# Kernel tuning notes

Hardware: AMD Instinct MI355X
Metric: run time of the kernel (lower is better)

Reference implementation:

```python
import jax, jax.numpy as jnp
import numpy as np

B, C, H, W = 16, 64, 128, 128
C8 = C // 8


def setup_inputs() -> dict:
    key = jax.random.key(0)
    ks = jax.random.split(key, 8)
    s = 0.05
    return {
        "x": jax.random.normal(ks[0], (B, C, H, W), dtype=jnp.float32),
        "Wq": jax.random.normal(ks[1], (C8, C), dtype=jnp.float32) * s,
        "bq": jax.random.normal(ks[2], (C8,), dtype=jnp.float32) * s,
        "Wk": jax.random.normal(ks[3], (C8, C), dtype=jnp.float32) * s,
        "bk": jax.random.normal(ks[4], (C8,), dtype=jnp.float32) * s,
        "Wv": jax.random.normal(ks[5], (C, C), dtype=jnp.float32) * s,
        "bv": jax.random.normal(ks[6], (C,), dtype=jnp.float32) * s,
        "gamma": jnp.zeros((1,), dtype=jnp.float32),
    }


def _criss_cross(x, Wq, bq, Wk, bk, Wv, bv, gamma):
    # 1x1 convs == channel-mixing matmuls
    q = jnp.einsum("bchw,oc->bohw", x, Wq) + bq[None, :, None, None]  # [B,C8,H,W]
    k = jnp.einsum("bchw,oc->bohw", x, Wk) + bk[None, :, None, None]  # [B,C8,H,W]
    v = jnp.einsum("bchw,oc->bohw", x, Wv) + bv[None, :, None, None]  # [B,C,H,W]

    h = x.shape[2]
    # column (H-axis) attention scores; diagonal masked to -inf
    energy_H = jnp.einsum("bchw,bciw->bhwi", q, k)  # [B,H,W,H]
    diag = jnp.eye(h, dtype=bool)[None, :, None, :]  # mask where query row == key row
    energy_H = jnp.where(diag, -jnp.inf, energy_H)
    # row (W-axis) attention scores
    energy_W = jnp.einsum("bchw,bchj->bhwj", q, k)  # [B,H,W,W]

    # joint softmax over concatenated H+W axis
    att = jax.nn.softmax(jnp.concatenate([energy_H, energy_W], axis=3), axis=3)
    att_H = att[:, :, :, :h]    # [B,H,W,H]
    att_W = att[:, :, :, h:]    # [B,H,W,W]

    out_H = jnp.einsum("bhwi,bciw->bchw", att_H, v)
    out_W = jnp.einsum("bhwj,bchj->bchw", att_W, v)
    return gamma[0] * (out_H + out_W) + x


def reference(x, Wq, bq, Wk, bk, Wv, bv, gamma):
    return _criss_cross(x, Wq, bq, Wk, bk, Wv, bv, gamma)
```

## Files before the change

kernel.cpp:

```cpp
#include <hip/hip_runtime.h>

#define HW 128
#define CC 64
#define C8V 8
#define NB 16
#define LOG2E 1.44269504088896f

typedef _Float16 h1;
typedef _Float16 h2 __attribute__((ext_vector_type(2)));
typedef _Float16 half8 __attribute__((ext_vector_type(8)));
typedef float float16v __attribute__((ext_vector_type(16)));
typedef uint uv4 __attribute__((ext_vector_type(4)));

__device__ __forceinline__ uint packh2(float a, float b) {
#if __has_builtin(__builtin_amdgcn_cvt_pkrtz)
  return __builtin_bit_cast(uint, __builtin_amdgcn_cvt_pkrtz(a, b));
#else
  h2 v; v[0] = (h1)a; v[1] = (h1)b; return __builtin_bit_cast(uint, v);
#endif
}
__device__ __forceinline__ ushort f2h(float a) { h1 v = (h1)a; return __builtin_bit_cast(ushort, v); }
__device__ __forceinline__ float  h2f(ushort a) { return (float)__builtin_bit_cast(h1, a); }

__device__ __forceinline__ float fexp2(float x) {
#if __has_builtin(__builtin_amdgcn_exp2f)
  return __builtin_amdgcn_exp2f(x);
#else
  return exp2f(x);
#endif
}

__device__ __forceinline__ float16v mfma16(uv4 a, uv4 b, float16v c) {
  return __builtin_amdgcn_mfma_f32_32x32x16_f16(
      __builtin_bit_cast(half8, a), __builtin_bit_cast(half8, b), c, 0, 0, 0);
}

__global__ __launch_bounds__(256) void k_prep(
    const float* __restrict__ Wq, const float* __restrict__ bq,
    const float* __restrict__ Wk, const float* __restrict__ bk,
    const float* __restrict__ Wv, const float* __restrict__ bv,
    ushort* __restrict__ W_frag, float* __restrict__ bias_f)
{
  int idx = blockIdx.x * 256 + threadIdx.x;
  if (idx < 6144) {
    int g = idx >> 3, e = idx & 7;
    int kshi = g / 96, o = g % 96;
    int ks = kshi >> 1, hi = kshi & 1;
    int c = 8 * hi + 16 * ks + e;
    float val = (o < 8)  ? Wq[o * 64 + c] * LOG2E
              : (o < 16) ? Wk[(o - 8) * 64 + c]
              : (o < 80) ? Wv[(o - 16) * 64 + c] : 0.f;
    W_frag[idx] = f2h(val);
  }
  if (blockIdx.x == 0 && threadIdx.x < 96) {
    int t = threadIdx.x;
    bias_f[t] = (t < 8) ? bq[t] * LOG2E : (t < 16) ? bk[t - 8] : (t < 80) ? bv[t - 16] : 0.f;
  }
}

__global__ __launch_bounds__(256, 4) void k_projW(
    const float* __restrict__ x, const ushort* __restrict__ W_frag,
    const float* __restrict__ bias_f,
    ushort* __restrict__ qT, ushort* __restrict__ kT,
    ushort* __restrict__ v,
    ushort* __restrict__ oW_, float* __restrict__ mW_, float* __restrict__ sW_)
{
  alignas(16) __shared__ uint V_l[64 * 64];
  alignas(16) __shared__ ushort qk_l[128 * 24];
  __shared__ float bias_l[96];

  int t = threadIdx.x;
  int lane = t & 63, wv = t >> 6, hi = lane >> 5;
  int b = blockIdx.x >> 7, r = blockIdx.x & 127;
  if (t < 96) bias_l[t] = bias_f[t];

  int w = 32 * wv + (lane & 31);
  const float* xw = x + (size_t)(b * CC) * (HW * HW) + (size_t)r * HW + w;
  const size_t PL = (size_t)HW * HW;

  float16v acc0 = {}, acc1 = {}, acc2 = {};
  #pragma unroll
  for (int ks = 0; ks < 4; ++ks) {
    int c0 = 8 * hi + 16 * ks;
    uint bx[4];
    #pragma unroll
    for (int e2 = 0; e2 < 4; ++e2) {
      float f0 = xw[(size_t)(c0 + 2 * e2) * PL];
      float f1 = xw[(size_t)(c0 + 2 * e2 + 1) * PL];
      bx[e2] = packh2(f0, f1);
    }
    uv4 Bx = {bx[0], bx[1], bx[2], bx[3]};
    const ushort* wf = W_frag + (size_t)(ks * 2 + hi) * 96 * 8;
    uv4 a0 = *(const uv4*)(wf + (lane & 31) * 8);
    uv4 a1 = *(const uv4*)(wf + ((lane & 31) + 32) * 8);
    uv4 a2 = *(const uv4*)(wf + ((lane & 31) + 64) * 8);
    acc0 = mfma16(a0, Bx, acc0);
    acc1 = mfma16(a1, Bx, acc1);
    acc2 = mfma16(a2, Bx, acc2);
  }
  __syncthreads();

  #pragma unroll
  for (int reg = 0; reg < 16; ++reg) {
    int orow = (reg & 3) + 8 * (reg >> 2) + 4 * hi;
    float v0 = acc0[reg] + bias_l[orow];
    if (orow < 16) {
      qk_l[w * 24 + orow] = f2h(v0);
    } else {
      int c = orow - 16;
      *(ushort*)((char*)V_l + c * 256 + ((2 * w) ^ ((c & 15) << 4))) = f2h(v0);
    }
    int c1 = orow + 16;
    *(ushort*)((char*)V_l + c1 * 256 + ((2 * w) ^ ((c1 & 15) << 4))) =
        f2h(acc1[reg] + bias_l[orow + 32]);
    if (orow < 16) {
      int c2_ = orow + 48;
      *(ushort*)((char*)V_l + c2_ * 256 + ((2 * w) ^ ((c2_ & 15) << 4))) =
          f2h(acc2[reg] + bias_l[orow + 64]);
    }
  }
  __syncthreads();

  ushort* vb = v + (size_t)(b * CC) * PL + (size_t)r * HW;
  #pragma unroll
  for (int i = 0; i < 4; ++i) {
    int idx = t + 256 * i; int c = idx >> 4, j8 = idx & 15;
    uv4 val = *(const uv4*)((const char*)V_l + c * 256 + ((16 * j8) ^ ((c & 15) << 4)));
    *(uv4*)(vb + (size_t)c * PL + j8 * 8) = val;
  }
  {
    int pix = t & 127, isk = t >> 7;
    uv4 val = *(const uv4*)&qk_l[pix * 24 + isk * 8];
    ushort* dstt = (isk ? kT : qT) + ((size_t)(b * HW + pix) * HW + r) * 8;
    *(uv4*)dstt = val;
  }

  int qg = w;
  uv4 Bq = {0, 0, 0, 0};
  uv4 ka[4] = {{0,0,0,0}, {0,0,0,0}, {0,0,0,0}, {0,0,0,0}};
  if (hi == 0) {
    Bq = *(const uv4*)&qk_l[qg * 24];
    #pragma unroll
    for (int mt = 0; mt < 4; ++mt)
      ka[mt] = *(const uv4*)&qk_l[((lane & 31) + 32 * mt) * 24 + 8];
  }

  float16v e[4];
  #pragma unroll
  for (int mt = 0; mt < 4; ++mt) {
    float16v z = {};
    e[mt] = mfma16(ka[mt], Bq, z);
  }

  float m = -INFINITY;
  #pragma unroll
  for (int mt = 0; mt < 4; ++mt)
    #pragma unroll
    for (int reg = 0; reg < 16; reg += 2)
      m = fmaxf(m, fmaxf(e[mt][reg], e[mt][reg + 1]));
  m = fmaxf(m, __shfl_xor(m, 32));

  float s0 = 0.f, s1 = 0.f, s2 = 0.f, s3 = 0.f;
  #pragma unroll
  for (int mt = 0; mt < 4; ++mt) {
    #pragma unroll
    for (int reg = 0; reg < 16; reg += 4) {
      float p0 = fexp2(e[mt][reg + 0] - m);
      float p1 = fexp2(e[mt][reg + 1] - m);
      float p2 = fexp2(e[mt][reg + 2] - m);
      float p3 = fexp2(e[mt][reg + 3] - m);
      e[mt][reg + 0] = p0; e[mt][reg + 1] = p1;
      e[mt][reg + 2] = p2; e[mt][reg + 3] = p3;
      s0 += p0; s1 += p1; s2 += p2; s3 += p3;
    }
  }
  float s = (s0 + s1) + (s2 + s3);
  s += __shfl_xor(s, 32);
  if (lane < 32) {
    mW_[(size_t)blockIdx.x * HW + qg] = m;
    sW_[(size_t)blockIdx.x * HW + qg] = s;
  }

  float16v pacc0 = {}, pacc1 = {};
  #pragma unroll
  for (int s8 = 0; s8 < 8; ++s8) {
    int mt = s8 >> 1, hf = s8 & 1;
    float p0 = e[mt][8 * hf + 0], p1 = e[mt][8 * hf + 1];
    float p2 = e[mt][8 * hf + 2], p3 = e[mt][8 * hf + 3];
    float p4 = e[mt][8 * hf + 4], p5 = e[mt][8 * hf + 5];
    float p6 = e[mt][8 * hf + 6], p7 = e[mt][8 * hf + 7];
    uint X = packh2(p0, p1), Y = packh2(p2, p3), Z = packh2(p4, p5), Wp = packh2(p6, p7);
    uint Xs = __shfl_xor(X, 32), Ys = __shfl_xor(Y, 32);
    uint Zs = __shfl_xor(Z, 32), Ws = __shfl_xor(Wp, 32);
    uv4 Bp;
    Bp[0] = (hi == 0) ? X  : Zs;
    Bp[1] = (hi == 0) ? Y  : Ws;
    Bp[2] = (hi == 0) ? Xs : Z;
    Bp[3] = (hi == 0) ? Ys : Wp;
    #pragma unroll
    for (int ct = 0; ct < 2; ++ct) {
      int c = (lane & 31) + 32 * ct;
      uint byteoff = c * 256 + ((16 * (hi + 2 * s8)) ^ ((c & 15) << 4));
      uv4 va = *(const uv4*)((const char*)V_l + byteoff);
      if (ct == 0) pacc0 = mfma16(va, Bp, pacc0);
      else         pacc1 = mfma16(va, Bp, pacc1);
    }
  }

  __syncthreads();
  ushort* o_l = (ushort*)V_l;
  #pragma unroll
  for (int reg = 0; reg < 16; ++reg) {
    int c = (reg & 3) + 8 * (reg >> 2) + 4 * hi;
    o_l[(c +  0) * 128 + w] = f2h(pacc0[reg]);
    o_l[(c + 32) * 128 + w] = f2h(pacc1[reg]);
  }
  __syncthreads();
  ushort* ob = oW_ + (size_t)(b * CC) * PL + (size_t)r * HW;
  #pragma unroll
  for (int i = 0; i < 4; ++i) {
    int idx = t + 256 * i; int c = idx >> 4, w8 = idx & 15;
    *(uv4*)(ob + (size_t)c * PL + w8 * 8) = *(const uv4*)&o_l[c * 128 + w8 * 8];
  }
}

__global__ __launch_bounds__(256) void k_transpose_v(const ushort* __restrict__ v,
                                                     ushort* __restrict__ vT)
{
  __shared__ ushort tl[128 * 130];
  int t = threadIdx.x;
  size_t base = (size_t)blockIdx.x * (HW * HW);
  const uint* ip = (const uint*)(v + base);
  uint* op = (uint*)(vT + base);
  int c2 = t & 63;
  int r0 = t >> 6;
  for (int it = 0; it < 32; ++it) {
    int r = it * 4 + r0;
    uint val = ip[r * 64 + c2];
    *(uint*)&tl[r * 130 + c2 * 2] = val;
  }
  __syncthreads();
  for (int it = 0; it < 32; ++it) {
    int wcol = it * 4 + r0;
    int hh = c2 * 2;
    uint lo = tl[hh * 130 + wcol];
    uint hi = tl[(hh + 1) * 130 + wcol];
    op[wcol * 64 + c2] = lo | (hi << 16);
  }
}

__global__ __launch_bounds__(256, 4) void k_attnH(
    const ushort* __restrict__ qT, const ushort* __restrict__ kT,
    const ushort* __restrict__ vT,
    ushort* __restrict__ oH_, float* __restrict__ mH_, float* __restrict__ sH_)
{
  alignas(16) __shared__ uint V_l[64 * 64];

  int t = threadIdx.x;
  int lane = t & 63, wv = t >> 6;
  int hi = lane >> 5;
  int bid = blockIdx.x;
  int b = bid >> 7, r = bid & 127;
  size_t plane32 = (size_t)(HW * HW) / 2;
  size_t pixbase = (size_t)(b * HW + r) * HW * 8;

  int qg = 32 * wv + (lane & 31);
  uv4 Bq = {0, 0, 0, 0};
  uv4 ka[4] = {{0,0,0,0}, {0,0,0,0}, {0,0,0,0}, {0,0,0,0}};
  if (hi == 0) {
    Bq = *(const uv4*)(qT + pixbase + (size_t)qg * 8);
    #pragma unroll
    for (int mt = 0; mt < 4; ++mt)
      ka[mt] = *(const uv4*)(kT + pixbase + (size_t)((lane & 31) + 32 * mt) * 8);
  }

  const uint* vrow = (const uint*)vT + (size_t)(b * CC) * plane32 + (size_t)r * 64;
  #pragma unroll
  for (int i = 0; i < 4; ++i) {
    int idx = t + 256 * i; int c = idx >> 4, j4 = idx & 15;
    uv4 val = *(const uv4*)(vrow + (size_t)c * plane32 + 4 * j4);
    uint byteoff = c * 256 + ((16 * j4) ^ ((c & 15) << 4));
    *(uv4*)((char*)V_l + byteoff) = val;
  }
  __syncthreads();

  float16v e[4];
  #pragma unroll
  for (int mt = 0; mt < 4; ++mt) {
    float16v z = {};
    e[mt] = mfma16(ka[mt], Bq, z);
  }

  #pragma unroll
  for (int mt = 0; mt < 4; ++mt)
    #pragma unroll
    for (int reg = 0; reg < 16; ++reg) {
      int key = 32 * mt + ((reg & 3) + 8 * (reg >> 2) + 4 * hi);
      e[mt][reg] = (key == qg) ? -INFINITY : e[mt][reg];
    }

  float m = -INFINITY;
  #pragma unroll
  for (int mt = 0; mt < 4; ++mt)
    #pragma unroll
    for (int reg = 0; reg < 16; reg += 2)
      m = fmaxf(m, fmaxf(e[mt][reg], e[mt][reg + 1]));
  m = fmaxf(m, __shfl_xor(m, 32));

  float s0 = 0.f, s1 = 0.f, s2 = 0.f, s3 = 0.f;
  #pragma unroll
  for (int mt = 0; mt < 4; ++mt) {
    #pragma unroll
    for (int reg = 0; reg < 16; reg += 4) {
      float p0 = fexp2(e[mt][reg + 0] - m);
      float p1 = fexp2(e[mt][reg + 1] - m);
      float p2 = fexp2(e[mt][reg + 2] - m);
      float p3 = fexp2(e[mt][reg + 3] - m);
      e[mt][reg + 0] = p0; e[mt][reg + 1] = p1;
      e[mt][reg + 2] = p2; e[mt][reg + 3] = p3;
      s0 += p0; s1 += p1; s2 += p2; s3 += p3;
    }
  }
  float s = (s0 + s1) + (s2 + s3);
  s += __shfl_xor(s, 32);
  if (lane < 32) {
    mH_[(size_t)bid * HW + qg] = m;
    sH_[(size_t)bid * HW + qg] = s;
  }

  float16v acc0 = {}, acc1 = {};
  #pragma unroll
  for (int s8 = 0; s8 < 8; ++s8) {
    int mt = s8 >> 1, hf = s8 & 1;
    float p0 = e[mt][8 * hf + 0], p1 = e[mt][8 * hf + 1];
    float p2 = e[mt][8 * hf + 2], p3 = e[mt][8 * hf + 3];
    float p4 = e[mt][8 * hf + 4], p5 = e[mt][8 * hf + 5];
    float p6 = e[mt][8 * hf + 6], p7 = e[mt][8 * hf + 7];
    uint X = packh2(p0, p1), Y = packh2(p2, p3), Z = packh2(p4, p5), Wp = packh2(p6, p7);
    uint Xs = __shfl_xor(X, 32), Ys = __shfl_xor(Y, 32);
    uint Zs = __shfl_xor(Z, 32), Ws = __shfl_xor(Wp, 32);
    uv4 Bp;
    Bp[0] = (hi == 0) ? X  : Zs;
    Bp[1] = (hi == 0) ? Y  : Ws;
    Bp[2] = (hi == 0) ? Xs : Z;
    Bp[3] = (hi == 0) ? Ys : Wp;
    #pragma unroll
    for (int ct = 0; ct < 2; ++ct) {
      int c = (lane & 31) + 32 * ct;
      uint byteoff = c * 256 + ((16 * (hi + 2 * s8)) ^ ((c & 15) << 4));
      uv4 va = *(const uv4*)((const char*)V_l + byteoff);
      if (ct == 0) acc0 = mfma16(va, Bp, acc0);
      else         acc1 = mfma16(va, Bp, acc1);
    }
  }

  __syncthreads();
  ushort* o_l = (ushort*)V_l;
  int w = 32 * wv + (lane & 31);
  #pragma unroll
  for (int reg = 0; reg < 16; ++reg) {
    int c = (reg & 3) + 8 * (reg >> 2) + 4 * hi;
    o_l[(c +  0) * 128 + w] = f2h(acc0[reg]);
    o_l[(c + 32) * 128 + w] = f2h(acc1[reg]);
  }
  __syncthreads();
  ushort* ob = oH_ + (size_t)(b * CC) * (HW * HW) + (size_t)r * HW;
  #pragma unroll
  for (int i = 0; i < 4; ++i) {
    int idx = t + 256 * i; int c = idx >> 4, w8 = idx & 15;
    *(uv4*)(ob + (size_t)c * (HW * HW) + w8 * 8) = *(const uv4*)&o_l[c * 128 + w8 * 8];
  }
}

__global__ __launch_bounds__(256) void k_alpha(
    const float* __restrict__ mH, const float* __restrict__ sH,
    const float* __restrict__ mW, const float* __restrict__ sW,
    ushort* __restrict__ aHT, ushort* __restrict__ aWn)
{
  __shared__ float mw_l[128 * 9], sw_l[128 * 9];
  __shared__ ushort aw_l[128 * 10];
  int t = threadIdx.x;
  int b = blockIdx.x >> 4, ws = blockIdx.x & 15;
  int w0 = ws * 8;
  const int PL = HW * HW;

  #pragma unroll
  for (int i = 0; i < 4; ++i) {
    int p = t + 256 * i;
    int w = p & 7, h = p >> 3;
    mw_l[h * 9 + w] = mW[(size_t)b * PL + h * HW + w0 + w];
    sw_l[h * 9 + w] = sW[(size_t)b * PL + h * HW + w0 + w];
  }
  __syncthreads();
  #pragma unroll
  for (int i = 0; i < 4; ++i) {
    int p = t + 256 * i;
    int h = p & 127, w = p >> 7;
    size_t tidx = (size_t)b * PL + (size_t)(w0 + w) * HW + h;
    float mh = mH[tidx], sh = sH[tidx];
    float mw = mw_l[h * 9 + w], sw = sw_l[h * 9 + w];
    float mm = fmaxf(mh, mw);
    float eh = fexp2(mh - mm), ew = fexp2(mw - mm);
    float inv = 1.f / (sh * eh + sw * ew);
    aHT[tidx] = f2h(eh * inv);
    aw_l[h * 10 + w] = f2h(ew * inv);
  }
  __syncthreads();
  #pragma unroll
  for (int i = 0; i < 4; ++i) {
    int p = t + 256 * i;
    int w = p & 7, h = p >> 3;
    aWn[(size_t)b * PL + (size_t)h * HW + w0 + w] = aw_l[h * 10 + w];
  }
}

__global__ __launch_bounds__(256) void k_merge(
    const ushort* __restrict__ oHT, const ushort* __restrict__ oW,
    const ushort* __restrict__ aHT, const ushort* __restrict__ aWn,
    const float* __restrict__ x, const float* __restrict__ gamma,
    float* __restrict__ out)
{
  alignas(16) __shared__ ushort otile[2 * 32 * 132];
  int t = threadIdx.x;
  int bid = blockIdx.x;
  int wsel = bid & 3, cg = (bid >> 2) & 31, b = bid >> 7;
  int w0 = wsel * 32;
  float g = gamma[0];
  const int PL = HW * HW;

  #pragma unroll
  for (int i = 0; i < 4; ++i) {
    int p = t + 256 * i;
    int ch = p >> 9, rest = p & 511;
    int w = rest >> 4, hg = rest & 15;
    size_t cbase = (size_t)(b * CC + cg * 2 + ch) * PL;
    uv4 ov = *(const uv4*)(oHT + cbase + (size_t)(w0 + w) * HW + hg * 8);
    uv4 av = *(const uv4*)(aHT + (size_t)b * PL + (size_t)(w0 + w) * HW + hg * 8);
    uv4 res;
    #pragma unroll
    for (int jj = 0; jj < 4; ++jj) {
      h2 o2 = __builtin_bit_cast(h2, ov[jj]);
      h2 a2 = __builtin_bit_cast(h2, av[jj]);
      res[jj] = __builtin_bit_cast(uint, o2 * a2);
    }
    *(uv4*)&otile[(ch * 32 + w) * 132 + hg * 8] = res;
  }
  __syncthreads();

  #pragma unroll
  for (int ch = 0; ch < 2; ++ch) {
    size_t cbase = (size_t)(b * CC + cg * 2 + ch) * PL;
    const ushort* otc = &otile[ch * 32 * 132];
    #pragma unroll
    for (int i = 0; i < 2; ++i) {
      int p = t + 256 * i;
      int w4 = p & 7, hh2 = p >> 3;
      float th0[4], th1[4];
      #pragma unroll
      for (int j = 0; j < 4; ++j) {
        uint pk = *(const uint*)&otc[(4 * w4 + j) * 132 + 2 * hh2];
        th0[j] = h2f((ushort)(pk & 0xffff));
        th1[j] = h2f((ushort)(pk >> 16));
      }
      #pragma unroll
      for (int rr = 0; rr < 2; ++rr) {
        int hh = 2 * hh2 + rr;
        const float* th = rr ? th1 : th0;
        size_t base = cbase + (size_t)hh * HW + w0 + 4 * w4;
        size_t abase = (size_t)b * PL + (size_t)hh * HW + w0 + 4 * w4;
        uint2 aw2 = *(const uint2*)(aWn + abase);
        uint2 ow2 = *(const uint2*)(oW + base);
        float4 xv = *(const float4*)(x + base);
        float4 res;
        res.x = g * (th[0] + h2f((ushort)(ow2.x & 0xffff)) * h2f((ushort)(aw2.x & 0xffff))) + xv.x;
        res.y = g * (th[1] + h2f((ushort)(ow2.x >> 16))    * h2f((ushort)(aw2.x >> 16)))    + xv.y;
        res.z = g * (th[2] + h2f((ushort)(ow2.y & 0xffff)) * h2f((ushort)(aw2.y & 0xffff))) + xv.z;
        res.w = g * (th[3] + h2f((ushort)(ow2.y >> 16))    * h2f((ushort)(aw2.y >> 16)))    + xv.w;
        *(float4*)(out + base) = res;
      }
    }
  }
}

extern "C" void kernel_launch(void* const* d_in, const int* in_sizes, int n_in,
                              void* d_out, int out_size, void* d_ws, size_t ws_size,
                              hipStream_t stream)
{
  const float* x     = (const float*)d_in[0];
  const float* Wq    = (const float*)d_in[1];
  const float* bq    = (const float*)d_in[2];
  const float* Wk    = (const float*)d_in[3];
  const float* bk    = (const float*)d_in[4];
  const float* Wv    = (const float*)d_in[5];
  const float* bv    = (const float*)d_in[6];
  const float* gamma = (const float*)d_in[7];
  float* out = (float*)d_out;

  char* w = (char*)d_ws;
  size_t np = (size_t)NB * HW * HW;
  ushort* W_frag = (ushort*)w; w += 6144 * 2;
  float*  bias_f = (float*)w;  w += 96 * 4 + 320;
  ushort* qT  = (ushort*)w;  w += np * 8 * 2;
  ushort* kT  = (ushort*)w;  w += np * 8 * 2;
  ushort* v   = (ushort*)w;  w += np * CC * 2;
  ushort* vT  = (ushort*)w;  w += np * CC * 2;
  ushort* oW  = (ushort*)w;  w += np * CC * 2;
  ushort* oHT = (ushort*)w;  w += np * CC * 2;
  float* mW = (float*)w;  w += np * 4;
  float* sW = (float*)w;  w += np * 4;
  float* mH = (float*)w;  w += np * 4;
  float* sH = (float*)w;  w += np * 4;
  ushort* aHT = (ushort*)w; w += np * 2;
  ushort* aWn = (ushort*)w; w += np * 2;
  if ((size_t)(w - (char*)d_ws) > ws_size) return;

  k_prep<<<24, 256, 0, stream>>>(Wq, bq, Wk, bk, Wv, bv, W_frag, bias_f);
  k_projW<<<NB * HW, 256, 0, stream>>>(x, W_frag, bias_f, qT, kT, v, oW, mW, sW);
  k_transpose_v<<<NB * CC, 256, 0, stream>>>(v, vT);
  k_attnH<<<NB * HW, 256, 0, stream>>>(qT, kT, vT, oHT, mH, sH);
  k_alpha<<<NB * 16, 256, 0, stream>>>(mH, sH, mW, sW, aHT, aWn);
  k_merge<<<NB * 32 * 4, 256, 0, stream>>>(oHT, oW, aHT, aWn, x, gamma, out);
}
```

Before: 107.4 us.

## Fuse softmax normalization into attnH and drop k_alpha kernel

Computes the joint H/W softmax combine factors directly inside k_attnH using the row-stats mW/sW, scales the H output by its weight before storing, and writes the W weight. This removes the separate k_alpha launch and the mH/sH/aHT buffers and their traffic, and lets k_merge skip the aHT load and multiply. It also hoists global loads in k_projW and k_merge ahead of compute to raise memory-level parallelism, at the cost of more registers. The mW/sW reads in attnH are strided gathers, one element per row.

After: 103.3 us. 1.04x faster.

```diff
diff --git a/kernel.cpp b/kernel.cpp
--- a/kernel.cpp
+++ b/kernel.cpp
@@ -2,7 +2,6 @@
 
 #define HW 128
 #define CC 64
-#define C8V 8
 #define NB 16
 #define LOG2E 1.44269504088896f
 
@@ -78,18 +77,23 @@
   const float* xw = x + (size_t)(b * CC) * (HW * HW) + (size_t)r * HW + w;
   const size_t PL = (size_t)HW * HW;
 
-  float16v acc0 = {}, acc1 = {}, acc2 = {};
+  float xv[32];
   #pragma unroll
   for (int ks = 0; ks < 4; ++ks) {
     int c0 = 8 * hi + 16 * ks;
-    uint bx[4];
-    #pragma unroll
-    for (int e2 = 0; e2 < 4; ++e2) {
-      float f0 = xw[(size_t)(c0 + 2 * e2) * PL];
-      float f1 = xw[(size_t)(c0 + 2 * e2 + 1) * PL];
-      bx[e2] = packh2(f0, f1);
-    }
-    uv4 Bx = {bx[0], bx[1], bx[2], bx[3]};
+    #pragma unroll
+    for (int e = 0; e < 8; ++e)
+      xv[ks * 8 + e] = xw[(size_t)(c0 + e) * PL];
+  }
+  __builtin_amdgcn_sched_barrier(0);
+
+  float16v acc0 = {}, acc1 = {}, acc2 = {};
+  #pragma unroll
+  for (int ks = 0; ks < 4; ++ks) {
+    uv4 Bx;
+    #pragma unroll
+    for (int e2 = 0; e2 < 4; ++e2)
+      Bx[e2] = packh2(xv[ks * 8 + 2 * e2], xv[ks * 8 + 2 * e2 + 1]);
     const ushort* wf = W_frag + (size_t)(ks * 2 + hi) * 96 * 8;
     uv4 a0 = *(const uv4*)(wf + (lane & 31) * 8);
     uv4 a1 = *(const uv4*)(wf + ((lane & 31) + 32) * 8);
@@ -252,7 +256,8 @@
 __global__ __launch_bounds__(256, 4) void k_attnH(
     const ushort* __restrict__ qT, const ushort* __restrict__ kT,
     const ushort* __restrict__ vT,
-    ushort* __restrict__ oH_, float* __restrict__ mH_, float* __restrict__ sH_)
+    const float* __restrict__ mW_, const float* __restrict__ sW_,
+    ushort* __restrict__ oH_, ushort* __restrict__ aWn)
 {
   alignas(16) __shared__ uint V_l[64 * 64];
 
@@ -262,6 +267,7 @@
   int bid = blockIdx.x;
   int b = bid >> 7, r = bid & 127;
   size_t plane32 = (size_t)(HW * HW) / 2;
+  const size_t PL = (size_t)HW * HW;
   size_t pixbase = (size_t)(b * HW + r) * HW * 8;
 
   int qg = 32 * wv + (lane & 31);
@@ -273,6 +279,8 @@
     for (int mt = 0; mt < 4; ++mt)
       ka[mt] = *(const uv4*)(kT + pixbase + (size_t)((lane & 31) + 32 * mt) * 8);
   }
+  float mw = mW_[(size_t)b * PL + (size_t)qg * HW + r];
+  float sw = sW_[(size_t)b * PL + (size_t)qg * HW + r];
 
   const uint* vrow = (const uint*)vT + (size_t)(b * CC) * plane32 + (size_t)r * 64;
   #pragma unroll
@@ -323,10 +331,13 @@
   }
   float s = (s0 + s1) + (s2 + s3);
   s += __shfl_xor(s, 32);
-  if (lane < 32) {
-    mH_[(size_t)bid * HW + qg] = m;
-    sH_[(size_t)bid * HW + qg] = s;
-  }
+
+  float mm = fmaxf(m, mw);
+  float eh = fexp2(m - mm), ew = fexp2(mw - mm);
+  float inv = 1.f / (s * eh + sw * ew);
+  float aH = eh * inv;
+  if (hi == 0)
+    aWn[(size_t)b * PL + (size_t)qg * HW + r] = f2h(ew * inv);
 
   float16v acc0 = {}, acc1 = {};
   #pragma unroll
@@ -360,63 +371,21 @@
   #pragma unroll
   for (int reg = 0; reg < 16; ++reg) {
     int c = (reg & 3) + 8 * (reg >> 2) + 4 * hi;
-    o_l[(c +  0) * 128 + w] = f2h(acc0[reg]);
-    o_l[(c + 32) * 128 + w] = f2h(acc1[reg]);
-  }
-  __syncthreads();
-  ushort* ob = oH_ + (size_t)(b * CC) * (HW * HW) + (size_t)r * HW;
+    o_l[(c +  0) * 128 + w] = f2h(acc0[reg] * aH);
+    o_l[(c + 32) * 128 + w] = f2h(acc1[reg] * aH);
+  }
+  __syncthreads();
+  ushort* ob = oH_ + (size_t)(b * CC) * PL + (size_t)r * HW;
   #pragma unroll
   for (int i = 0; i < 4; ++i) {
     int idx = t + 256 * i; int c = idx >> 4, w8 = idx & 15;
-    *(uv4*)(ob + (size_t)c * (HW * HW) + w8 * 8) = *(const uv4*)&o_l[c * 128 + w8 * 8];
-  }
-}
-
-__global__ __launch_bounds__(256) void k_alpha(
-    const float* __restrict__ mH, const float* __restrict__ sH,
-    const float* __restrict__ mW, const float* __restrict__ sW,
-    ushort* __restrict__ aHT, ushort* __restrict__ aWn)
-{
-  __shared__ float mw_l[128 * 9], sw_l[128 * 9];
-  __shared__ ushort aw_l[128 * 10];
-  int t = threadIdx.x;
-  int b = blockIdx.x >> 4, ws = blockIdx.x & 15;
-  int w0 = ws * 8;
-  const int PL = HW * HW;
-
-  #pragma unroll
-  for (int i = 0; i < 4; ++i) {
-    int p = t + 256 * i;
-    int w = p & 7, h = p >> 3;
-    mw_l[h * 9 + w] = mW[(size_t)b * PL + h * HW + w0 + w];
-    sw_l[h * 9 + w] = sW[(size_t)b * PL + h * HW + w0 + w];
-  }
-  __syncthreads();
-  #pragma unroll
-  for (int i = 0; i < 4; ++i) {
-    int p = t + 256 * i;
-    int h = p & 127, w = p >> 7;
-    size_t tidx = (size_t)b * PL + (size_t)(w0 + w) * HW + h;
-    float mh = mH[tidx], sh = sH[tidx];
-    float mw = mw_l[h * 9 + w], sw = sw_l[h * 9 + w];
-    float mm = fmaxf(mh, mw);
-    float eh = fexp2(mh - mm), ew = fexp2(mw - mm);
-    float inv = 1.f / (sh * eh + sw * ew);
-    aHT[tidx] = f2h(eh * inv);
-    aw_l[h * 10 + w] = f2h(ew * inv);
-  }
-  __syncthreads();
-  #pragma unroll
-  for (int i = 0; i < 4; ++i) {
-    int p = t + 256 * i;
-    int w = p & 7, h = p >> 3;
-    aWn[(size_t)b * PL + (size_t)h * HW + w0 + w] = aw_l[h * 10 + w];
+    *(uv4*)(ob + (size_t)c * PL + w8 * 8) = *(const uv4*)&o_l[c * 128 + w8 * 8];
   }
 }
 
 __global__ __launch_bounds__(256) void k_merge(
     const ushort* __restrict__ oHT, const ushort* __restrict__ oW,
-    const ushort* __restrict__ aHT, const ushort* __restrict__ aWn,
+    const ushort* __restrict__ aWn,
     const float* __restrict__ x, const float* __restrict__ gamma,
     float* __restrict__ out)
 {
@@ -428,22 +397,39 @@
   float g = gamma[0];
   const int PL = HW * HW;
 
+  uv4 ov[4];
   #pragma unroll
   for (int i = 0; i < 4; ++i) {
     int p = t + 256 * i;
     int ch = p >> 9, rest = p & 511;
     int w = rest >> 4, hg = rest & 15;
     size_t cbase = (size_t)(b * CC + cg * 2 + ch) * PL;
-    uv4 ov = *(const uv4*)(oHT + cbase + (size_t)(w0 + w) * HW + hg * 8);
-    uv4 av = *(const uv4*)(aHT + (size_t)b * PL + (size_t)(w0 + w) * HW + hg * 8);
-    uv4 res;
-    #pragma unroll
-    for (int jj = 0; jj < 4; ++jj) {
-      h2 o2 = __builtin_bit_cast(h2, ov[jj]);
-      h2 a2 = __builtin_bit_cast(h2, av[jj]);
-      res[jj] = __builtin_bit_cast(uint, o2 * a2);
-    }
-    *(uv4*)&otile[(ch * 32 + w) * 132 + hg * 8] = res;
+    ov[i] = *(const uv4*)(oHT + cbase + (size_t)(w0 + w) * HW + hg * 8);
+  }
+  uint2 owp[8]; float4 xp[8]; uint2 awp[4];
+  #pragma unroll
+  for (int i = 0; i < 2; ++i) {
+    int p = t + 256 * i;
+    int w4 = p & 7, hh2 = p >> 3;
+    #pragma unroll
+    for (int rr = 0; rr < 2; ++rr) {
+      int hh = 2 * hh2 + rr;
+      size_t poff = (size_t)hh * HW + w0 + 4 * w4;
+      awp[i * 2 + rr] = *(const uint2*)(aWn + (size_t)b * PL + poff);
+      #pragma unroll
+      for (int ch = 0; ch < 2; ++ch) {
+        size_t base = (size_t)(b * CC + cg * 2 + ch) * PL + poff;
+        owp[ch * 4 + i * 2 + rr] = *(const uint2*)(oW + base);
+        xp[ch * 4 + i * 2 + rr]  = *(const float4*)(x + base);
+      }
+    }
+  }
+  #pragma unroll
+  for (int i = 0; i < 4; ++i) {
+    int p = t + 256 * i;
+    int ch = p >> 9, rest = p & 511;
+    int w = rest >> 4, hg = rest & 15;
+    *(uv4*)&otile[(ch * 32 + w) * 132 + hg * 8] = ov[i];
   }
   __syncthreads();
 
@@ -467,10 +453,9 @@
         int hh = 2 * hh2 + rr;
         const float* th = rr ? th1 : th0;
         size_t base = cbase + (size_t)hh * HW + w0 + 4 * w4;
-        size_t abase = (size_t)b * PL + (size_t)hh * HW + w0 + 4 * w4;
-        uint2 aw2 = *(const uint2*)(aWn + abase);
-        uint2 ow2 = *(const uint2*)(oW + base);
-        float4 xv = *(const float4*)(x + base);
+        uint2 aw2 = awp[i * 2 + rr];
+        uint2 ow2 = owp[ch * 4 + i * 2 + rr];
+        float4 xv = xp[ch * 4 + i * 2 + rr];
         float4 res;
         res.x = g * (th[0] + h2f((ushort)(ow2.x & 0xffff)) * h2f((ushort)(aw2.x & 0xffff))) + xv.x;
         res.y = g * (th[1] + h2f((ushort)(ow2.x >> 16))    * h2f((ushort)(aw2.x >> 16)))    + xv.y;
@@ -508,16 +493,12 @@
   ushort* oHT = (ushort*)w;  w += np * CC * 2;
   float* mW = (float*)w;  w += np * 4;
   float* sW = (float*)w;  w += np * 4;
-  float* mH = (float*)w;  w += np * 4;
-  float* sH = (float*)w;  w += np * 4;
-  ushort* aHT = (ushort*)w; w += np * 2;
   ushort* aWn = (ushort*)w; w += np * 2;
   if ((size_t)(w - (char*)d_ws) > ws_size) return;
 
   k_prep<<<24, 256, 0, stream>>>(Wq, bq, Wk, bk, Wv, bv, W_frag, bias_f);
   k_projW<<<NB * HW, 256, 0, stream>>>(x, W_frag, bias_f, qT, kT, v, oW, mW, sW);
   k_transpose_v<<<NB * CC, 256, 0, stream>>>(v, vT);
-  k_attnH<<<NB * HW, 256, 0, stream>>>(qT, kT, vT, oHT, mH, sH);
-  k_alpha<<<NB * 16, 256, 0, stream>>>(mH, sH, mW, sW, aHT, aWn);
-  k_merge<<<NB * 32 * 4, 256, 0, stream>>>(oHT, oW, aHT, aWn, x, gamma, out);
-}
+  k_attnH<<<NB * HW, 256, 0, stream>>>(qT, kT, vT, mW, sW, oHT, aWn);
+  k_merge<<<NB * 32 * 4, 256, 0, stream>>>(oHT, oW, aWn, x, gamma, out);
+}
```
